# Optimization experiments

Measured on AMD Instinct MI355X. Metric: run time of the kernel, lower is better.

## Reference

```python
import jax, jax.numpy as jnp
import numpy as np

N = 50000
E = 800000
IN_C = 1024
HID = 64
HEADS = 4
OUT_C = 64
NEG_SLOPE = 0.2  # PyG GATConv default


def setup_inputs() -> dict:
    key = jax.random.key(0)
    ks = jax.random.split(key, 12)
    x = jax.random.normal(ks[0], (N, IN_C), dtype=jnp.float32)
    edge_index = jax.random.randint(ks[1], (2, E), 0, N, dtype=jnp.int64)
    s1 = 1.0 / np.sqrt(IN_C)
    s2 = 1.0 / np.sqrt(HEADS * HID)
    return {
        "x": x,
        "edge_index": edge_index,
        "W1": jax.random.normal(ks[2], (HEADS * HID, IN_C), dtype=jnp.float32) * s1,
        "a_src1": jax.random.normal(ks[3], (HEADS, HID), dtype=jnp.float32) * s2,
        "a_dst1": jax.random.normal(ks[4], (HEADS, HID), dtype=jnp.float32) * s2,
        "b1": jnp.zeros((HEADS * HID,), dtype=jnp.float32),
        "W2": jax.random.normal(ks[5], (OUT_C, HEADS * HID), dtype=jnp.float32) * s2,
        "a_src2": jax.random.normal(ks[6], (1, OUT_C), dtype=jnp.float32) * 0.1,
        "a_dst2": jax.random.normal(ks[7], (1, OUT_C), dtype=jnp.float32) * 0.1,
        "b2": jnp.zeros((OUT_C,), dtype=jnp.float32),
    }


def gat_conv(x, src, dst, W, a_src, a_dst, b, heads, concat):
    # x: [N, F_in]; src/dst: [E'] (self-loops already appended)
    n = x.shape[0]
    h = (x @ W.T).reshape(n, heads, -1)                 # [N, H, C]
    alpha_s = (h * a_src).sum(-1)                       # [N, H]
    alpha_d = (h * a_dst).sum(-1)                       # [N, H]
    e = jax.nn.leaky_relu(alpha_s[src] + alpha_d[dst], NEG_SLOPE)  # [E', H]
    # segment softmax over edges grouped by destination
    m = jax.ops.segment_max(e, dst, num_segments=n)     # [N, H]
    ex = jnp.exp(e - m[dst])
    denom = jax.ops.segment_sum(ex, dst, num_segments=n)
    alpha = ex / denom[dst]                             # [E', H]
    out = jax.ops.segment_sum(alpha[:, :, None] * h[src], dst, num_segments=n)  # [N, H, C]
    out = out.reshape(n, -1) if concat else out.mean(axis=1)
    return out + b


def reference(x, edge_index, W1, a_src1, a_dst1, b1, W2, a_src2, a_dst2, b2):
    n = x.shape[0]
    loop = jnp.arange(n, dtype=edge_index.dtype)
    src = jnp.concatenate([edge_index[0], loop])  # PyG add_self_loops=True
    dst = jnp.concatenate([edge_index[1], loop])
    # eval mode: dropout is identity
    h = gat_conv(x, src, dst, W1, a_src1, a_dst1, b1, HEADS, concat=True)
    h = jax.nn.elu(h)
    out = gat_conv(h, src, dst, W2, a_src2, a_dst2, b2, 1, concat=False)
    return out
```

## Files before the change

kernel.cpp:

```cpp
#include <hip/hip_runtime.h>
#include <hip/hip_bf16.h>
#include <math.h>

constexpr int IN_C = 1024;
constexpr int HEADS = 4;
constexpr int F1 = 256;
constexpr int OUT_C = 64;
constexpr float NEG = 0.2f;

using bf16x8 = __attribute__((ext_vector_type(8))) short;
using f32x4 = __attribute__((ext_vector_type(4))) float;

__device__ __forceinline__ float leaky(float x) { return x > 0.f ? x : NEG * x; }

__device__ __forceinline__ unsigned short bf16bits(float v) {
  __hip_bfloat16 b = __float2bfloat16(v);
  return *reinterpret_cast<unsigned short*>(&b);
}
__device__ __forceinline__ float bf2f(unsigned short u) {
  union { unsigned u; float f; } c; c.u = (unsigned)u << 16; return c.f;
}

#define GLD_LDS16(g, l)                                                        \
  __builtin_amdgcn_global_load_lds(                                            \
      (const __attribute__((address_space(1))) void*)(g),                      \
      (__attribute__((address_space(3))) void*)(l), 16, 0, 0)

constexpr int NB_W1 = (F1 * IN_C) / 256;
constexpr int NB_W2 = (OUT_C * F1) / 256;

__global__ __launch_bounds__(256) void prep_kernel(const float* __restrict__ W1,
                                                   unsigned short* __restrict__ W1b,
                                                   const float* __restrict__ W2,
                                                   unsigned short* __restrict__ W2b,
                                                   const int* __restrict__ ei, int E, int N,
                                                   int* __restrict__ deg) {
  int b = blockIdx.x;
  if (b < NB_W1) {
    int i = b * 256 + threadIdx.x;
    W1b[i] = bf16bits(W1[i]);
  } else if (b < NB_W1 + NB_W2) {
    int i = (b - NB_W1) * 256 + threadIdx.x;
    W2b[i] = bf16bits(W2[i]);
  } else {
    int e = (b - NB_W1 - NB_W2) * 256 + threadIdx.x;
    if (e < E + N) {
      int dst = (e < E) ? ei[E + e] : (e - E);
      atomicAdd(&deg[dst], 1);
    }
  }
}

constexpr int LDTA = 72;

__global__ __launch_bounds__(256, 2) void gemm1_mfma(const float* __restrict__ X,
                                                     const unsigned short* __restrict__ Wb,
                                                     unsigned short* __restrict__ Hb,
                                                     const float* __restrict__ a_src,
                                                     const float* __restrict__ a_dst,
                                                     float* __restrict__ as_out,
                                                     float* __restrict__ ad_out, int M) {
  __shared__ unsigned short As[64 * LDTA];
  __shared__ unsigned short Bs[256 * 64];
  const int tid = threadIdx.x;
  const int wave = tid >> 6;
  const int lane = tid & 63;
  const int m15 = lane & 15;
  const int q = lane >> 4;
  const int bm = blockIdx.x * 64;

  f32x4 acc[4][4];
#pragma unroll
  for (int i = 0; i < 4; ++i)
#pragma unroll
    for (int j = 0; j < 4; ++j) acc[i][j] = (f32x4){0.f, 0.f, 0.f, 0.f};

  const int ar = tid >> 2;
  const int acg = (tid & 3) * 16;
  const int agr = (bm + ar < M) ? (bm + ar) : (M - 1);
  const float* aptr = X + (size_t)agr * IN_C + acg;

  for (int kt = 0; kt < IN_C; kt += 64) {
    float4 a0 = *(const float4*)(aptr + kt + 0);
    float4 a1 = *(const float4*)(aptr + kt + 4);
    float4 a2 = *(const float4*)(aptr + kt + 8);
    float4 a3 = *(const float4*)(aptr + kt + 12);
#pragma unroll
    for (int p = 0; p < 8; ++p) {
      int s = p * 256 + tid;
      int r = s >> 3;
      int cb = s & 7;
      const unsigned short* g = Wb + (size_t)r * IN_C + kt + ((cb ^ (r & 7)) << 3);
      GLD_LDS16(g, &Bs[(p * 256 + wave * 64) * 8]);
    }
    union { uint4 u4[2]; __hip_bfloat162 h[8]; } pk;
    pk.h[0] = __float22bfloat162_rn(make_float2(a0.x, a0.y));
    pk.h[1] = __float22bfloat162_rn(make_float2(a0.z, a0.w));
    pk.h[2] = __float22bfloat162_rn(make_float2(a1.x, a1.y));
    pk.h[3] = __float22bfloat162_rn(make_float2(a1.z, a1.w));
    pk.h[4] = __float22bfloat162_rn(make_float2(a2.x, a2.y));
    pk.h[5] = __float22bfloat162_rn(make_float2(a2.z, a2.w));
    pk.h[6] = __float22bfloat162_rn(make_float2(a3.x, a3.y));
    pk.h[7] = __float22bfloat162_rn(make_float2(a3.z, a3.w));
    *(uint4*)&As[ar * LDTA + acg] = pk.u4[0];
    *(uint4*)&As[ar * LDTA + acg + 8] = pk.u4[1];
    __syncthreads();

#pragma unroll
    for (int k0 = 0; k0 < 64; k0 += 32) {
      bf16x8 af[4], bfr[4];
#pragma unroll
      for (int i = 0; i < 4; ++i)
        af[i] = *(const bf16x8*)&As[(i * 16 + m15) * LDTA + k0 + q * 8];
#pragma unroll
      for (int j = 0; j < 4; ++j) {
        int rb = wave * 64 + j * 16 + m15;
        int cbp = ((k0 >> 3) + q) ^ (rb & 7);
        bfr[j] = *(const bf16x8*)&Bs[rb * 64 + cbp * 8];
      }
#pragma unroll
      for (int i = 0; i < 4; ++i)
#pragma unroll
        for (int j = 0; j < 4; ++j)
          acc[i][j] = __builtin_amdgcn_mfma_f32_16x16x32_bf16(af[i], bfr[j], acc[i][j], 0, 0, 0);
    }
    __syncthreads();
  }
  float asf[4], adf[4];
#pragma unroll
  for (int j = 0; j < 4; ++j) {
    asf[j] = a_src[wave * 64 + j * 16 + m15];
    adf[j] = a_dst[wave * 64 + j * 16 + m15];
  }
#pragma unroll
  for (int i = 0; i < 4; ++i) {
#pragma unroll
    for (int r = 0; r < 4; ++r) {
      int row = bm + i * 16 + q * 4 + r;
      if (row < M) {
#pragma unroll
        for (int j = 0; j < 4; ++j)
          Hb[(size_t)row * F1 + wave * 64 + j * 16 + m15] = bf16bits(acc[i][j][r]);
      }
      float s = acc[i][0][r] * asf[0] + acc[i][1][r] * asf[1] +
                acc[i][2][r] * asf[2] + acc[i][3][r] * asf[3];
      float d = acc[i][0][r] * adf[0] + acc[i][1][r] * adf[1] +
                acc[i][2][r] * adf[2] + acc[i][3][r] * adf[3];
#pragma unroll
      for (int o = 1; o < 16; o <<= 1) {
        s += __shfl_xor(s, o, 64);
        d += __shfl_xor(d, o, 64);
      }
      if (m15 == 0 && row < M) {
        as_out[row * HEADS + wave] = s;
        ad_out[row * HEADS + wave] = d;
      }
    }
  }
}

__global__ __launch_bounds__(256, 4) void gemm2_mfma(const unsigned short* __restrict__ Y,
                                                     const unsigned short* __restrict__ W2b,
                                                     float* __restrict__ H2,
                                                     const float* __restrict__ a_src,
                                                     const float* __restrict__ a_dst,
                                                     float* __restrict__ as_out,
                                                     float* __restrict__ ad_out, int M) {
  __shared__ unsigned short As[64 * 64];
  __shared__ unsigned short Bs[64 * 64];
  const int tid = threadIdx.x;
  const int wave = tid >> 6;
  const int lane = tid & 63;
  const int m15 = lane & 15;
  const int q = lane >> 4;
  const int bm = blockIdx.x * 64;

  f32x4 acc[4];
#pragma unroll
  for (int j = 0; j < 4; ++j) acc[j] = (f32x4){0.f, 0.f, 0.f, 0.f};

  for (int kt = 0; kt < F1; kt += 64) {
#pragma unroll
    for (int p = 0; p < 2; ++p) {
      int s = p * 256 + tid;
      int r = s >> 3;
      int cb = s & 7;
      int colo = (cb ^ (r & 7)) << 3;
      int gr = (bm + r < M) ? (bm + r) : (M - 1);
      GLD_LDS16(Y + (size_t)gr * F1 + kt + colo, &As[(p * 256 + wave * 64) * 8]);
      GLD_LDS16(W2b + (size_t)r * F1 + kt + colo, &Bs[(p * 256 + wave * 64) * 8]);
    }
    __syncthreads();
#pragma unroll
    for (int k0 = 0; k0 < 64; k0 += 32) {
      int ra = wave * 16 + m15;
      bf16x8 af = *(const bf16x8*)&As[ra * 64 + ((((k0 >> 3) + q) ^ (ra & 7)) << 3)];
      bf16x8 bfr[4];
#pragma unroll
      for (int j = 0; j < 4; ++j) {
        int rb = j * 16 + m15;
        bfr[j] = *(const bf16x8*)&Bs[rb * 64 + ((((k0 >> 3) + q) ^ (rb & 7)) << 3)];
      }
#pragma unroll
      for (int j = 0; j < 4; ++j)
        acc[j] = __builtin_amdgcn_mfma_f32_16x16x32_bf16(af, bfr[j], acc[j], 0, 0, 0);
    }
    __syncthreads();
  }
  float asf[4], adf[4];
#pragma unroll
  for (int j = 0; j < 4; ++j) {
    asf[j] = a_src[j * 16 + m15];
    adf[j] = a_dst[j * 16 + m15];
  }
#pragma unroll
  for (int r = 0; r < 4; ++r) {
    int row = bm + wave * 16 + q * 4 + r;
    if (row < M) {
#pragma unroll
      for (int j = 0; j < 4; ++j) H2[(size_t)row * OUT_C + j * 16 + m15] = acc[j][r];
    }
    float s = acc[0][r] * asf[0] + acc[1][r] * asf[1] + acc[2][r] * asf[2] + acc[3][r] * asf[3];
    float d = acc[0][r] * adf[0] + acc[1][r] * adf[1] + acc[2][r] * adf[2] + acc[3][r] * adf[3];
#pragma unroll
    for (int o = 1; o < 16; o <<= 1) {
      s += __shfl_xor(s, o, 64);
      d += __shfl_xor(d, o, 64);
    }
    if (m15 == 0 && row < M) {
      as_out[row] = s;
      ad_out[row] = d;
    }
  }
}

__global__ __launch_bounds__(256) void scan_block_sums(const int* __restrict__ deg,
                                                       int* __restrict__ part, int n) {
  __shared__ int sm[256];
  int t = threadIdx.x;
  int i = blockIdx.x * 256 + t;
  sm[t] = (i < n) ? deg[i] : 0;
  __syncthreads();
  for (int off = 128; off > 0; off >>= 1) {
    if (t < off) sm[t] += sm[t + off];
    __syncthreads();
  }
  if (t == 0) part[blockIdx.x] = sm[0];
}

__global__ __launch_bounds__(256) void scan_final2(const int* __restrict__ deg,
                                                   const int* __restrict__ part,
                                                   int* __restrict__ row_ptr, int n) {
  __shared__ int sm[256];
  __shared__ int wsum[4];
  int t = threadIdx.x;
  int i = blockIdx.x * 256 + t;
  sm[t] = (i < n) ? deg[i] : 0;
  int pv = (t < blockIdx.x) ? part[t] : 0;
#pragma unroll
  for (int o = 1; o < 64; o <<= 1) pv += __shfl_xor(pv, o, 64);
  if ((t & 63) == 0) wsum[t >> 6] = pv;
  __syncthreads();
  for (int off = 1; off < 256; off <<= 1) {
    int u = (t >= off) ? sm[t - off] : 0;
    __syncthreads();
    sm[t] += u;
    __syncthreads();
  }
  int base = wsum[0] + wsum[1] + wsum[2] + wsum[3];
  if (i < n) row_ptr[i + 1] = base + sm[t];
  if (i == 0) row_ptr[0] = 0;
}

__global__ void scatter_kernel(const int* __restrict__ ei, int E, int N,
                               const int* __restrict__ row_ptr, int* __restrict__ fill,
                               int* __restrict__ col) {
  int e = blockIdx.x * blockDim.x + threadIdx.x;
  if (e >= E + N) return;
  int src, dst;
  if (e < E) { src = ei[e]; dst = ei[E + e]; }
  else       { src = e - E; dst = e - E; }
  int pos = row_ptr[dst] + atomicAdd(&fill[dst], 1);
  col[pos] = src;
}

__global__ __launch_bounds__(256) void agg1_kernel(const unsigned short* __restrict__ hb,
                                                   const float* __restrict__ as,
                                                   const float* __restrict__ ad,
                                                   const int* __restrict__ row_ptr,
                                                   const int* __restrict__ col,
                                                   const float* __restrict__ bias,
                                                   unsigned short* __restrict__ yb, int N) {
  int dst = (blockIdx.x * blockDim.x + threadIdx.x) >> 6;
  int lane = threadIdx.x & 63;
  if (dst >= N) return;
  const int s0 = row_ptr[dst], s1 = row_ptr[dst + 1];
  const int par = lane >> 5;
  const int cg = lane & 31;
  const int hh = cg >> 3;
  const float adl = ad[dst * 4 + hh];
  float acc[8];
#pragma unroll
  for (int k = 0; k < 8; ++k) acc[k] = 0.f;
  float den = 0.f;

  int i = s0 + par;
  for (; i + 6 < s1; i += 8) {
    int sA = col[i], sB = col[i + 2], sC = col[i + 4], sD = col[i + 6];
    float wA = __expf(leaky(as[sA * 4 + hh] + adl));
    float wB = __expf(leaky(as[sB * 4 + hh] + adl));
    float wC = __expf(leaky(as[sC * 4 + hh] + adl));
    float wD = __expf(leaky(as[sD * 4 + hh] + adl));
    uint4 hA = *(const uint4*)(hb + (size_t)sA * F1 + cg * 8);
    uint4 hB = *(const uint4*)(hb + (size_t)sB * F1 + cg * 8);
    uint4 hC = *(const uint4*)(hb + (size_t)sC * F1 + cg * 8);
    uint4 hD = *(const uint4*)(hb + (size_t)sD * F1 + cg * 8);
    den += (wA + wB) + (wC + wD);
    const unsigned short* pa = (const unsigned short*)&hA;
    const unsigned short* pb = (const unsigned short*)&hB;
    const unsigned short* pc = (const unsigned short*)&hC;
    const unsigned short* pd = (const unsigned short*)&hD;
#pragma unroll
    for (int k = 0; k < 8; ++k) {
      acc[k] = fmaf(wA, bf2f(pa[k]), acc[k]);
      acc[k] = fmaf(wB, bf2f(pb[k]), acc[k]);
      acc[k] = fmaf(wC, bf2f(pc[k]), acc[k]);
      acc[k] = fmaf(wD, bf2f(pd[k]), acc[k]);
    }
  }
  for (; i + 2 < s1; i += 4) {
    int sA = col[i], sB = col[i + 2];
    float wA = __expf(leaky(as[sA * 4 + hh] + adl));
    float wB = __expf(leaky(as[sB * 4 + hh] + adl));
    uint4 hA = *(const uint4*)(hb + (size_t)sA * F1 + cg * 8);
    uint4 hB = *(const uint4*)(hb + (size_t)sB * F1 + cg * 8);
    den += wA + wB;
    const unsigned short* pa = (const unsigned short*)&hA;
    const unsigned short* pb = (const unsigned short*)&hB;
#pragma unroll
    for (int k = 0; k < 8; ++k) {
      acc[k] = fmaf(wA, bf2f(pa[k]), acc[k]);
      acc[k] = fmaf(wB, bf2f(pb[k]), acc[k]);
    }
  }
  for (; i < s1; i += 2) {
    int s = col[i];
    float w = __expf(leaky(as[s * 4 + hh] + adl));
    uint4 hv = *(const uint4*)(hb + (size_t)s * F1 + cg * 8);
    den += w;
    const unsigned short* p = (const unsigned short*)&hv;
#pragma unroll
    for (int k = 0; k < 8; ++k) acc[k] = fmaf(w, bf2f(p[k]), acc[k]);
  }
  den += __shfl_xor(den, 32, 64);
#pragma unroll
  for (int k = 0; k < 8; ++k) acc[k] += __shfl_xor(acc[k], 32, 64);

  if (par == 0) {
    const float iv = 1.f / den;
    float4 b0 = *(const float4*)(bias + cg * 8);
    float4 b1 = *(const float4*)(bias + cg * 8 + 4);
    float bv[8] = {b0.x, b0.y, b0.z, b0.w, b1.x, b1.y, b1.z, b1.w};
    ushort4 o[2];
    unsigned short* po = (unsigned short*)o;
#pragma unroll
    for (int k = 0; k < 8; ++k) {
      float v = acc[k] * iv + bv[k];
      v = v > 0.f ? v : (__expf(v) - 1.f);
      po[k] = bf16bits(v);
    }
    *(uint4*)(yb + (size_t)dst * F1 + cg * 8) = *(uint4*)o;
  }
}

__global__ __launch_bounds__(256) void agg2_kernel(const float* __restrict__ h,
                                                   const float* __restrict__ as,
                                                   const float* __restrict__ ad,
                                                   const int* __restrict__ row_ptr,
                                                   const int* __restrict__ col,
                                                   const float* __restrict__ bias,
                                                   float* __restrict__ out, int N) {
  int dst = (blockIdx.x * blockDim.x + threadIdx.x) >> 6;
  int lane = threadIdx.x & 63;
  if (dst >= N) return;
  const int s0 = row_ptr[dst], s1 = row_ptr[dst + 1];
  const int par = lane >> 5;
  const int cg = lane & 31;
  const float adl = ad[dst];
  float a0 = 0.f, a1 = 0.f, den = 0.f;

  int i = s0 + par;
  for (; i + 6 < s1; i += 8) {
    int sA = col[i], sB = col[i + 2], sC = col[i + 4], sD = col[i + 6];
    float wA = __expf(leaky(as[sA] + adl));
    float wB = __expf(leaky(as[sB] + adl));
    float wC = __expf(leaky(as[sC] + adl));
    float wD = __expf(leaky(as[sD] + adl));
    float2 hA = *(const float2*)(h + (size_t)sA * OUT_C + cg * 2);
    float2 hB = *(const float2*)(h + (size_t)sB * OUT_C + cg * 2);
    float2 hC = *(const float2*)(h + (size_t)sC * OUT_C + cg * 2);
    float2 hD = *(const float2*)(h + (size_t)sD * OUT_C + cg * 2);
    den += (wA + wB) + (wC + wD);
    a0 = fmaf(wA, hA.x, a0); a1 = fmaf(wA, hA.y, a1);
    a0 = fmaf(wB, hB.x, a0); a1 = fmaf(wB, hB.y, a1);
    a0 = fmaf(wC, hC.x, a0); a1 = fmaf(wC, hC.y, a1);
    a0 = fmaf(wD, hD.x, a0); a1 = fmaf(wD, hD.y, a1);
  }
  for (; i + 2 < s1; i += 4) {
    int sA = col[i], sB = col[i + 2];
    float wA = __expf(leaky(as[sA] + adl));
    float wB = __expf(leaky(as[sB] + adl));
    float2 hA = *(const float2*)(h + (size_t)sA * OUT_C + cg * 2);
    float2 hB = *(const float2*)(h + (size_t)sB * OUT_C + cg * 2);
    den += wA + wB;
    a0 = fmaf(wA, hA.x, a0); a1 = fmaf(wA, hA.y, a1);
    a0 = fmaf(wB, hB.x, a0); a1 = fmaf(wB, hB.y, a1);
  }
  for (; i < s1; i += 2) {
    int s = col[i];
    float w = __expf(leaky(as[s] + adl));
    float2 hv = *(const float2*)(h + (size_t)s * OUT_C + cg * 2);
    den += w;
    a0 = fmaf(w, hv.x, a0); a1 = fmaf(w, hv.y, a1);
  }
  den += __shfl_xor(den, 32, 64);
  a0 += __shfl_xor(a0, 32, 64);
  a1 += __shfl_xor(a1, 32, 64);
  if (par == 0) {
    const float iv = 1.f / den;
    float2 bv = *(const float2*)(bias + cg * 2);
    float2 o = make_float2(a0 * iv + bv.x, a1 * iv + bv.y);
    *(float2*)(out + (size_t)dst * OUT_C + cg * 2) = o;
  }
}

extern "C" void kernel_launch(void* const* d_in, const int* in_sizes, int n_in,
                              void* d_out, int out_size, void* d_ws, size_t ws_size,
                              hipStream_t stream) {
  const float* x      = (const float*)d_in[0];
  const int*   ei     = (const int*)d_in[1];
  const float* W1     = (const float*)d_in[2];
  const float* a_src1 = (const float*)d_in[3];
  const float* a_dst1 = (const float*)d_in[4];
  const float* b1     = (const float*)d_in[5];
  const float* W2     = (const float*)d_in[6];
  const float* a_src2 = (const float*)d_in[7];
  const float* a_dst2 = (const float*)d_in[8];
  const float* b2     = (const float*)d_in[9];
  float* out = (float*)d_out;

  const int N = in_sizes[0] / IN_C;
  const int E = in_sizes[1] / 2;
  const int ET = E + N;

  char* ws = (char*)d_ws;
  size_t off = 0;
  auto alloc = [&](size_t bytes) -> void* {
    void* p = ws + off;
    off = (off + bytes + 255) & ~(size_t)255;
    return p;
  };
  unsigned short* h1b = (unsigned short*)alloc((size_t)N * F1 * 2);
  unsigned short* y1b = (unsigned short*)alloc((size_t)N * F1 * 2);
  float* h2      = (float*)alloc((size_t)N * OUT_C * 4);
  float* as1     = (float*)alloc((size_t)N * HEADS * 4);
  float* ad1     = (float*)alloc((size_t)N * HEADS * 4);
  float* as2     = (float*)alloc((size_t)N * 4);
  float* ad2     = (float*)alloc((size_t)N * 4);
  int*   deg     = (int*)alloc((size_t)N * 2 * 4);
  int*   fill    = deg + N;
  int*   row_ptr = (int*)alloc((size_t)(N + 1) * 4);
  int*   col     = (int*)alloc((size_t)ET * 4);
  int*   part    = (int*)alloc(1024 * 4);
  unsigned short* W1b = (unsigned short*)alloc((size_t)F1 * IN_C * 2);
  unsigned short* W2b = (unsigned short*)alloc((size_t)OUT_C * F1 * 2);
  (void)off; (void)ws_size; (void)n_in; (void)out_size;

  hipMemsetAsync(deg, 0, (size_t)N * 2 * 4, stream);

  const int NBD = (ET + 255) / 256;
  const int P = (N + 255) / 256;

  prep_kernel<<<NB_W1 + NB_W2 + NBD, 256, 0, stream>>>(W1, W1b, W2, W2b, ei, E, N, deg);
  scan_block_sums<<<P, 256, 0, stream>>>(deg, part, N);
  scan_final2<<<P, 256, 0, stream>>>(deg, part, row_ptr, N);
  scatter_kernel<<<NBD, 256, 0, stream>>>(ei, E, N, row_ptr, fill, col);

  const int NB4 = (N + 3) / 4;

  gemm1_mfma<<<(N + 63) / 64, 256, 0, stream>>>(x, W1b, h1b, a_src1, a_dst1, as1, ad1, N);
  agg1_kernel<<<NB4, 256, 0, stream>>>(h1b, as1, ad1, row_ptr, col, b1, y1b, N);

  gemm2_mfma<<<(N + 63) / 64, 256, 0, stream>>>(y1b, W2b, h2, a_src2, a_dst2, as2, ad2, N);
  agg2_kernel<<<NB4, 256, 0, stream>>>(h2, as2, ad2, row_ptr, col, b2, out, N);
}
```

Measured before the change: 522.9 us.

## Widen gemm1 to 128-row tiles and fold edge scatter into its launch

After: 490.7 us. 6.2% less time.

```diff
diff --git a/kernel.cpp b/kernel.cpp
--- a/kernel.cpp
+++ b/kernel.cpp
@@ -53,21 +53,41 @@
 
 constexpr int LDTA = 72;
 
-__global__ __launch_bounds__(256, 2) void gemm1_mfma(const float* __restrict__ X,
+__global__ __launch_bounds__(512, 4) void gemm1_mfma(const float* __restrict__ X,
                                                      const unsigned short* __restrict__ Wb,
                                                      unsigned short* __restrict__ Hb,
                                                      const float* __restrict__ a_src,
                                                      const float* __restrict__ a_dst,
                                                      float* __restrict__ as_out,
-                                                     float* __restrict__ ad_out, int M) {
-  __shared__ unsigned short As[64 * LDTA];
+                                                     float* __restrict__ ad_out, int M, int MB,
+                                                     const int* __restrict__ ei, int E, int N,
+                                                     const int* __restrict__ row_ptr,
+                                                     int* __restrict__ fill,
+                                                     int* __restrict__ col) {
+  __shared__ unsigned short As[128 * LDTA];
   __shared__ unsigned short Bs[256 * 64];
   const int tid = threadIdx.x;
+
+  if (blockIdx.x >= MB) {
+    int e = (blockIdx.x - MB) * 512 + tid;
+    int ET = E + N;
+    if (e < ET) {
+      int src, dst;
+      if (e < E) { src = ei[e]; dst = ei[E + e]; }
+      else       { src = e - E; dst = e - E; }
+      int pos = row_ptr[dst] + atomicAdd(&fill[dst], 1);
+      col[pos] = src;
+    }
+    return;
+  }
+
   const int wave = tid >> 6;
   const int lane = tid & 63;
   const int m15 = lane & 15;
   const int q = lane >> 4;
-  const int bm = blockIdx.x * 64;
+  const int rg = wave >> 2;
+  const int cg4 = wave & 3;
+  const int bm = blockIdx.x * 128;
 
   f32x4 acc[4][4];
 #pragma unroll
@@ -86,12 +106,12 @@
     float4 a2 = *(const float4*)(aptr + kt + 8);
     float4 a3 = *(const float4*)(aptr + kt + 12);
 #pragma unroll
-    for (int p = 0; p < 8; ++p) {
-      int s = p * 256 + tid;
+    for (int p = 0; p < 4; ++p) {
+      int s = p * 512 + tid;
       int r = s >> 3;
       int cb = s & 7;
       const unsigned short* g = Wb + (size_t)r * IN_C + kt + ((cb ^ (r & 7)) << 3);
-      GLD_LDS16(g, &Bs[(p * 256 + wave * 64) * 8]);
+      GLD_LDS16(g, &Bs[(p * 512 + wave * 64) * 8]);
     }
     union { uint4 u4[2]; __hip_bfloat162 h[8]; } pk;
     pk.h[0] = __float22bfloat162_rn(make_float2(a0.x, a0.y));
@@ -111,10 +131,10 @@
       bf16x8 af[4], bfr[4];
 #pragma unroll
       for (int i = 0; i < 4; ++i)
-        af[i] = *(const bf16x8*)&As[(i * 16 + m15) * LDTA + k0 + q * 8];
+        af[i] = *(const bf16x8*)&As[(rg * 64 + i * 16 + m15) * LDTA + k0 + q * 8];
 #pragma unroll
       for (int j = 0; j < 4; ++j) {
-        int rb = wave * 64 + j * 16 + m15;
+        int rb = cg4 * 64 + j * 16 + m15;
         int cbp = ((k0 >> 3) + q) ^ (rb & 7);
         bfr[j] = *(const bf16x8*)&Bs[rb * 64 + cbp * 8];
       }
@@ -129,18 +149,18 @@
   float asf[4], adf[4];
 #pragma unroll
   for (int j = 0; j < 4; ++j) {
-    asf[j] = a_src[wave * 64 + j * 16 + m15];
-    adf[j] = a_dst[wave * 64 + j * 16 + m15];
+    asf[j] = a_src[cg4 * 64 + j * 16 + m15];
+    adf[j] = a_dst[cg4 * 64 + j * 16 + m15];
   }
 #pragma unroll
   for (int i = 0; i < 4; ++i) {
 #pragma unroll
     for (int r = 0; r < 4; ++r) {
-      int row = bm + i * 16 + q * 4 + r;
+      int row = bm + rg * 64 + i * 16 + q * 4 + r;
       if (row < M) {
 #pragma unroll
         for (int j = 0; j < 4; ++j)
-          Hb[(size_t)row * F1 + wave * 64 + j * 16 + m15] = bf16bits(acc[i][j][r]);
+          Hb[(size_t)row * F1 + cg4 * 64 + j * 16 + m15] = bf16bits(acc[i][j][r]);
       }
       float s = acc[i][0][r] * asf[0] + acc[i][1][r] * asf[1] +
                 acc[i][2][r] * asf[2] + acc[i][3][r] * asf[3];
@@ -152,8 +172,8 @@
         d += __shfl_xor(d, o, 64);
       }
       if (m15 == 0 && row < M) {
-        as_out[row * HEADS + wave] = s;
-        ad_out[row * HEADS + wave] = d;
+        as_out[row * HEADS + cg4] = s;
+        ad_out[row * HEADS + cg4] = d;
       }
     }
   }
@@ -270,18 +290,6 @@
   int base = wsum[0] + wsum[1] + wsum[2] + wsum[3];
   if (i < n) row_ptr[i + 1] = base + sm[t];
   if (i == 0) row_ptr[0] = 0;
-}
-
-__global__ void scatter_kernel(const int* __restrict__ ei, int E, int N,
-                               const int* __restrict__ row_ptr, int* __restrict__ fill,
-                               int* __restrict__ col) {
-  int e = blockIdx.x * blockDim.x + threadIdx.x;
-  if (e >= E + N) return;
-  int src, dst;
-  if (e < E) { src = ei[e]; dst = ei[E + e]; }
-  else       { src = e - E; dst = e - E; }
-  int pos = row_ptr[dst] + atomicAdd(&fill[dst], 1);
-  col[pos] = src;
 }
 
 __global__ __launch_bounds__(256) void agg1_kernel(const unsigned short* __restrict__ hb,
@@ -484,11 +492,13 @@
   prep_kernel<<<NB_W1 + NB_W2 + NBD, 256, 0, stream>>>(W1, W1b, W2, W2b, ei, E, N, deg);
   scan_block_sums<<<P, 256, 0, stream>>>(deg, part, N);
   scan_final2<<<P, 256, 0, stream>>>(deg, part, row_ptr, N);
-  scatter_kernel<<<NBD, 256, 0, stream>>>(ei, E, N, row_ptr, fill, col);
 
   const int NB4 = (N + 3) / 4;
-
-  gemm1_mfma<<<(N + 63) / 64, 256, 0, stream>>>(x, W1b, h1b, a_src1, a_dst1, as1, ad1, N);
+  const int MB = (N + 127) / 128;
+  const int SB = (ET + 511) / 512;
+
+  gemm1_mfma<<<MB + SB, 512, 0, stream>>>(x, W1b, h1b, a_src1, a_dst1, as1, ad1, N, MB,
+                                          ei, E, N, row_ptr, fill, col);
   agg1_kernel<<<NB4, 256, 0, stream>>>(h1b, as1, ad1, row_ptr, col, b1, y1b, N);
 
   gemm2_mfma<<<(N + 63) / 64, 256, 0, stream>>>(y1b, W2b, h2, a_src2, a_dst2, as2, ad2, N);
```

## Fold CSR scatter into gemm1 launch and prefetch next X tile

Applied to the files above, without the earlier changes.

New measurement: 515.6 us. Within noise of the previous version (-1.4%).

```diff
diff --git a/kernel.cpp b/kernel.cpp
--- a/kernel.cpp
+++ b/kernel.cpp
@@ -53,16 +53,34 @@
 
 constexpr int LDTA = 72;
 
-__global__ __launch_bounds__(256, 2) void gemm1_mfma(const float* __restrict__ X,
+__global__ __launch_bounds__(256, 3) void gemm1_mfma(const float* __restrict__ X,
                                                      const unsigned short* __restrict__ Wb,
                                                      unsigned short* __restrict__ Hb,
                                                      const float* __restrict__ a_src,
                                                      const float* __restrict__ a_dst,
                                                      float* __restrict__ as_out,
-                                                     float* __restrict__ ad_out, int M) {
+                                                     float* __restrict__ ad_out, int M, int MB,
+                                                     const int* __restrict__ ei, int E, int N,
+                                                     const int* __restrict__ row_ptr,
+                                                     int* __restrict__ fill,
+                                                     int* __restrict__ col) {
   __shared__ unsigned short As[64 * LDTA];
   __shared__ unsigned short Bs[256 * 64];
   const int tid = threadIdx.x;
+
+  if (blockIdx.x >= MB) {
+    int e = (blockIdx.x - MB) * 256 + tid;
+    int ET = E + N;
+    if (e < ET) {
+      int src, dst;
+      if (e < E) { src = ei[e]; dst = ei[E + e]; }
+      else       { src = e - E; dst = e - E; }
+      int pos = row_ptr[dst] + atomicAdd(&fill[dst], 1);
+      col[pos] = src;
+    }
+    return;
+  }
+
   const int wave = tid >> 6;
   const int lane = tid & 63;
   const int m15 = lane & 15;
@@ -80,11 +98,12 @@
   const int agr = (bm + ar < M) ? (bm + ar) : (M - 1);
   const float* aptr = X + (size_t)agr * IN_C + acg;
 
+  float4 a0 = *(const float4*)(aptr + 0);
+  float4 a1 = *(const float4*)(aptr + 4);
+  float4 a2 = *(const float4*)(aptr + 8);
+  float4 a3 = *(const float4*)(aptr + 12);
+
   for (int kt = 0; kt < IN_C; kt += 64) {
-    float4 a0 = *(const float4*)(aptr + kt + 0);
-    float4 a1 = *(const float4*)(aptr + kt + 4);
-    float4 a2 = *(const float4*)(aptr + kt + 8);
-    float4 a3 = *(const float4*)(aptr + kt + 12);
 #pragma unroll
     for (int p = 0; p < 8; ++p) {
       int s = p * 256 + tid;
@@ -104,6 +123,12 @@
     pk.h[7] = __float22bfloat162_rn(make_float2(a3.z, a3.w));
     *(uint4*)&As[ar * LDTA + acg] = pk.u4[0];
     *(uint4*)&As[ar * LDTA + acg + 8] = pk.u4[1];
+    if (kt + 64 < IN_C) {
+      a0 = *(const float4*)(aptr + kt + 64 + 0);
+      a1 = *(const float4*)(aptr + kt + 64 + 4);
+      a2 = *(const float4*)(aptr + kt + 64 + 8);
+      a3 = *(const float4*)(aptr + kt + 64 + 12);
+    }
     __syncthreads();
 
 #pragma unroll
@@ -270,18 +295,6 @@
   int base = wsum[0] + wsum[1] + wsum[2] + wsum[3];
   if (i < n) row_ptr[i + 1] = base + sm[t];
   if (i == 0) row_ptr[0] = 0;
-}
-
-__global__ void scatter_kernel(const int* __restrict__ ei, int E, int N,
-                               const int* __restrict__ row_ptr, int* __restrict__ fill,
-                               int* __restrict__ col) {
-  int e = blockIdx.x * blockDim.x + threadIdx.x;
-  if (e >= E + N) return;
-  int src, dst;
-  if (e < E) { src = ei[e]; dst = ei[E + e]; }
-  else       { src = e - E; dst = e - E; }
-  int pos = row_ptr[dst] + atomicAdd(&fill[dst], 1);
-  col[pos] = src;
 }
 
 __global__ __launch_bounds__(256) void agg1_kernel(const unsigned short* __restrict__ hb,
@@ -484,11 +497,13 @@
   prep_kernel<<<NB_W1 + NB_W2 + NBD, 256, 0, stream>>>(W1, W1b, W2, W2b, ei, E, N, deg);
   scan_block_sums<<<P, 256, 0, stream>>>(deg, part, N);
   scan_final2<<<P, 256, 0, stream>>>(deg, part, row_ptr, N);
-  scatter_kernel<<<NBD, 256, 0, stream>>>(ei, E, N, row_ptr, fill, col);
 
   const int NB4 = (N + 3) / 4;
-
-  gemm1_mfma<<<(N + 63) / 64, 256, 0, stream>>>(x, W1b, h1b, a_src1, a_dst1, as1, ad1, N);
+  const int MB = (N + 63) / 64;
+  const int SB = (ET + 255) / 256;
+
+  gemm1_mfma<<<MB + SB, 256, 0, stream>>>(x, W1b, h1b, a_src1, a_dst1, as1, ad1, N, MB,
+                                          ei, E, N, row_ptr, fill, col);
   agg1_kernel<<<NB4, 256, 0, stream>>>(h1b, as1, ad1, row_ptr, col, b1, y1b, N);
 
   gemm2_mfma<<<(N + 63) / 64, 256, 0, stream>>>(y1b, W2b, h2, a_src2, a_dst2, as2, ad2, N);
```
